# Kernel optimization log

Hardware: AMD Instinct MI355X
Metric: run time of the kernel (lower is better)

## Reference

```python
import jax, jax.numpy as jnp
import numpy as np

PATCH = 3
ALPHA = 0.5
EPS = 1e-12  # F.normalize default eps


def _unfold(x, p):
    # nn.Unfold(kernel_size=p, padding=p//2) then reshape(B, C, p*p, H*W)
    B, C, H, W = x.shape
    pad = p // 2
    xp = jnp.pad(x, ((0, 0), (0, 0), (pad, pad), (pad, pad)))
    # kernel positions row-major, matching torch unfold channel-major layout
    pats = jnp.stack([xp[:, :, i:i + H, j:j + W]
                      for i in range(p) for j in range(p)], axis=2)  # [B,C,K,H,W]
    return pats.reshape(B, C, p * p, H * W)


def setup_inputs() -> dict:
    key = jax.random.key(0)
    k1, k2 = jax.random.split(key)
    B, C, H, W = 4, 32, 256, 256
    fe_lv = jax.random.normal(k1, (B, C, H, W), dtype=jnp.float32)
    fused_features = jax.random.normal(k2, (B, C, H, W), dtype=jnp.float32)
    return {"fe_lv": fe_lv, "fused_features": fused_features}


def reference(fe_lv, fused_features):
    B, C, H, W = fe_lv.shape
    N = H * W
    patches = _unfold(fused_features, PATCH)          # [B,C,K,N]
    fe_flat = fe_lv.reshape(B, C, N)                  # [B,C,N]

    # cosine similarity over channel dim
    pn = patches / jnp.maximum(jnp.linalg.norm(patches, axis=1, keepdims=True), EPS)
    fn = fe_flat / jnp.maximum(jnp.linalg.norm(fe_flat, axis=1, keepdims=True), EPS)
    cosine_sim = jnp.einsum('bckn,bcn->bnk', pn, fn)  # [B,N,K]
    cosine_weights = jax.nn.softmax(cosine_sim, axis=-1)

    # euclidean distance over channel dim
    dist = jnp.sqrt(jnp.sum((patches - fe_flat[:, :, None, :]) ** 2, axis=1))  # [B,K,N]
    euclidean_weights = jax.nn.softmax(-dist.transpose(0, 2, 1), axis=-1)      # [B,N,K]

    weights = ALPHA * cosine_weights + (1.0 - ALPHA) * euclidean_weights
    refined = jnp.einsum('bnk,bckn->bcn', weights, patches)  # [B,C,N]
    return refined.reshape(B, C, H, W) + fe_lv
```

## Files before the change

kernel.cpp:

```cpp
#include <hip/hip_runtime.h>
#include <math.h>

#define B_ 4
#define C_ 32
#define H_ 256
#define W_ 256
#define HW_ (H_ * W_)
#define K_ 9
#define TX 32
#define TY 4
#define HX 34
#define HY 6
#define HCH (HX * HY)
#define NOCT 4
#define EPS_ 1e-12f

typedef _Float16 h2v __attribute__((ext_vector_type(2)));
typedef _Float16 h8v __attribute__((ext_vector_type(8)));

#if defined(__has_builtin)
#if __has_builtin(__builtin_amdgcn_fdot2)
#define HAVE_FDOT2 1
#endif
#if __has_builtin(__builtin_amdgcn_cvt_pkrtz)
#define HAVE_PKRTZ 1
#endif
#endif

static __device__ __forceinline__ h2v pk2(float a, float b) {
#if defined(HAVE_PKRTZ)
    return __builtin_bit_cast(h2v, __builtin_amdgcn_cvt_pkrtz(a, b));
#else
    h2v r = {(_Float16)a, (_Float16)b};
    return r;
#endif
}

static __device__ __forceinline__ float dot2(h2v a, h2v b, float c) {
#if defined(HAVE_FDOT2)
    return __builtin_amdgcn_fdot2(a, b, c, false);
#else
    return c + (float)a[0] * (float)b[0] + (float)a[1] * (float)b[1];
#endif
}

__global__ __launch_bounds__(256, 6) void asfr_kernel(const float* __restrict__ fe,
                                                      const float* __restrict__ fu,
                                                      float* __restrict__ out) {
    __shared__ h8v lds8[NOCT * 256];
    const int t = threadIdx.x;
    const int bx = blockIdx.x & 7;
    const int by = (blockIdx.x >> 3) & 63;
    const int b  = blockIdx.x >> 9;
    const int w0 = bx * TX, h0 = by * TY;

    const int x = t & 31;
    const int half = (t >> 5) & 1;
    const int y = t >> 6;
    const int c0 = half << 4;
    const int pxoff = b * (C_ * HW_) + (h0 + y) * W_ + (w0 + x);

    int goff[4];
    float msk[4];
#pragma unroll
    for (int j = 0; j < 4; ++j) {
        int u = t + j * 256;
        int oct = u >> 8;
        int pos = u & 255;
        int pp = pos < HCH ? pos : HCH - 1;
        int r = pp / HX;
        int col = pp - r * HX;
        int hh = h0 - 1 + r;
        int ww = w0 - 1 + col;
        bool ok = (pos < HCH) && ((unsigned)hh < (unsigned)H_) && ((unsigned)ww < (unsigned)W_);
        int hcl = hh < 0 ? 0 : (hh > H_ - 1 ? H_ - 1 : hh);
        int wcl = ww < 0 ? 0 : (ww > W_ - 1 ? W_ - 1 : ww);
        goff[j] = (oct * 8) * HW_ + hcl * W_ + wcl;
        msk[j] = ok ? 1.f : 0.f;
    }

    float fv[16];
#pragma unroll
    for (int cc = 0; cc < 16; ++cc) fv[cc] = fe[pxoff + (c0 + cc) * HW_];
    h8v fe8[2];
#pragma unroll
    for (int j = 0; j < 2; ++j)
#pragma unroll
        for (int c = 0; c < 4; ++c) {
            h2v p = pk2(fv[8 * j + 2 * c], fv[8 * j + 2 * c + 1]);
            fe8[j][2 * c] = p[0];
            fe8[j][2 * c + 1] = p[1];
        }

    const float* fub = fu + b * (C_ * HW_);
    float s[32];
#pragma unroll
    for (int j = 0; j < 4; ++j)
#pragma unroll
        for (int c = 0; c < 8; ++c) s[8 * j + c] = fub[goff[j] + c * HW_];
#pragma unroll
    for (int j = 0; j < 4; ++j) {
        h8v hv;
#pragma unroll
        for (int c = 0; c < 4; ++c) {
            h2v p = pk2(s[8 * j + 2 * c] * msk[j], s[8 * j + 2 * c + 1] * msk[j]);
            hv[2 * c] = p[0];
            hv[2 * c + 1] = p[1];
        }
        lds8[t + j * 256] = hv;
    }
    __syncthreads();

    const int hc = (y + 1) * HX + (x + 1);
    const int koff[K_] = {-HX - 1, -HX, -HX + 1, -1, 0, 1, HX - 1, HX, HX + 1};

    float dot[K_], psq[K_];
#pragma unroll
    for (int k = 0; k < K_; ++k) { dot[k] = 0.f; psq[k] = 0.f; }
    float fsq = 0.f;

#pragma unroll
    for (int j = 0; j < 2; ++j) {
        const int oct = 2 * half + j;
        h8v fq = fe8[j];
        h2v fA0 = __builtin_shufflevector(fq, fq, 0, 1);
        h2v fA1 = __builtin_shufflevector(fq, fq, 2, 3);
        h2v fA2 = __builtin_shufflevector(fq, fq, 4, 5);
        h2v fA3 = __builtin_shufflevector(fq, fq, 6, 7);
        fsq = dot2(fA0, fA0, fsq);
        fsq = dot2(fA1, fA1, fsq);
        fsq = dot2(fA2, fA2, fsq);
        fsq = dot2(fA3, fA3, fsq);
        const h8v* fubase = &lds8[(oct << 8) + hc];
#pragma unroll
        for (int k = 0; k < K_; ++k) {
            h8v p8 = fubase[koff[k]];
            h2v p0 = __builtin_shufflevector(p8, p8, 0, 1);
            h2v p1 = __builtin_shufflevector(p8, p8, 2, 3);
            h2v p2 = __builtin_shufflevector(p8, p8, 4, 5);
            h2v p3 = __builtin_shufflevector(p8, p8, 6, 7);
            dot[k] = dot2(p0, fA0, dot[k]);
            dot[k] = dot2(p1, fA1, dot[k]);
            dot[k] = dot2(p2, fA2, dot[k]);
            dot[k] = dot2(p3, fA3, dot[k]);
            psq[k] = dot2(p0, p0, psq[k]);
            psq[k] = dot2(p1, p1, psq[k]);
            psq[k] = dot2(p2, p2, psq[k]);
            psq[k] = dot2(p3, p3, psq[k]);
        }
    }

#pragma unroll
    for (int k = 0; k < K_; ++k) {
        dot[k] += __shfl_xor(dot[k], 32);
        psq[k] += __shfl_xor(psq[k], 32);
    }
    fsq += __shfl_xor(fsq, 32);

    float nf = fmaxf(sqrtf(fsq), EPS_);
    float cosv[K_], negd[K_];
#pragma unroll
    for (int k = 0; k < K_; ++k) {
        float np = fmaxf(sqrtf(psq[k]), EPS_);
        cosv[k] = __fdividef(dot[k], np * nf);
        float dsq = fmaxf(psq[k] - 2.f * dot[k] + fsq, 0.f);
        negd[k] = -sqrtf(dsq);
    }

    float m1 = cosv[0], m2 = negd[0];
#pragma unroll
    for (int k = 1; k < K_; ++k) { m1 = fmaxf(m1, cosv[k]); m2 = fmaxf(m2, negd[k]); }
    float s1 = 0.f, s2 = 0.f, e1[K_], e2[K_];
#pragma unroll
    for (int k = 0; k < K_; ++k) {
        e1[k] = __expf(cosv[k] - m1);
        e2[k] = __expf(negd[k] - m2);
        s1 += e1[k]; s2 += e2[k];
    }
    float r1 = __fdividef(0.5f, s1), r2 = __fdividef(0.5f, s2);
    h2v w2[K_];
#pragma unroll
    for (int k = 0; k < K_; ++k) {
        float wk = fmaf(e1[k], r1, e2[k] * r2);
        _Float16 wh = (_Float16)wk;
        h2v tmp = {wh, wh};
        w2[k] = tmp;
    }

#pragma unroll
    for (int j = 0; j < 2; ++j) {
        const int oct = 2 * half + j;
        const h8v* fubase = &lds8[(oct << 8) + hc];
        h2v a0 = {(_Float16)0, (_Float16)0};
        h2v a1 = a0, a2 = a0, a3 = a0;
#pragma unroll
        for (int k = 0; k < K_; ++k) {
            h8v p8 = fubase[koff[k]];
            a0 += w2[k] * __builtin_shufflevector(p8, p8, 0, 1);
            a1 += w2[k] * __builtin_shufflevector(p8, p8, 2, 3);
            a2 += w2[k] * __builtin_shufflevector(p8, p8, 4, 5);
            a3 += w2[k] * __builtin_shufflevector(p8, p8, 6, 7);
        }
        h8v fq = fe8[j];
        const int cg = oct * 8;
        out[pxoff + (cg + 0) * HW_] = (float)(fq[0] + a0[0]);
        out[pxoff + (cg + 1) * HW_] = (float)(fq[1] + a0[1]);
        out[pxoff + (cg + 2) * HW_] = (float)(fq[2] + a1[0]);
        out[pxoff + (cg + 3) * HW_] = (float)(fq[3] + a1[1]);
        out[pxoff + (cg + 4) * HW_] = (float)(fq[4] + a2[0]);
        out[pxoff + (cg + 5) * HW_] = (float)(fq[5] + a2[1]);
        out[pxoff + (cg + 6) * HW_] = (float)(fq[6] + a3[0]);
        out[pxoff + (cg + 7) * HW_] = (float)(fq[7] + a3[1]);
    }
}

extern "C" void kernel_launch(void* const* d_in, const int* in_sizes, int n_in,
                              void* d_out, int out_size, void* d_ws, size_t ws_size,
                              hipStream_t stream) {
    const float* fe = (const float*)d_in[0];
    const float* fu = (const float*)d_in[1];
    float* out = (float*)d_out;
    dim3 grid((W_ / TX) * (H_ / TY) * B_), block(256);
    hipLaunchKernelGGL(asfr_kernel, grid, block, 0, stream, fe, fu, out);
}
```

Before: 32.07 us.

## Precompute per-pixel patch squared norms in LDS and use rsqrt for cosine

Each halo pixel's squared norm over all 32 channels is computed once in fp32 while staging, stored in a shared buffer, and read back for the 9 neighbours. This removes the per-neighbour psq dot2 accumulation and its cross-half shuffle. The halo load is reorganized so each thread fetches all 32 channels of one spatial position, and the fe norm is computed in fp32. Cosine normalization now uses a single rsqrt of the product of squared norms instead of two sqrts and a divide. The cost is slightly different epsilon clamping and extra LDS space.

```diff
diff --git a/kernel.cpp b/kernel.cpp
--- a/kernel.cpp
+++ b/kernel.cpp
@@ -25,6 +25,13 @@
 #if __has_builtin(__builtin_amdgcn_cvt_pkrtz)
 #define HAVE_PKRTZ 1
 #endif
+#if __has_builtin(__builtin_amdgcn_rsqf)
+#define RSQ(xx) __builtin_amdgcn_rsqf(xx)
+#else
+#define RSQ(xx) (1.0f / sqrtf(xx))
+#endif
+#else
+#define RSQ(xx) (1.0f / sqrtf(xx))
 #endif
 
 static __device__ __forceinline__ h2v pk2(float a, float b) {
@@ -48,6 +55,7 @@
                                                       const float* __restrict__ fu,
                                                       float* __restrict__ out) {
     __shared__ h8v lds8[NOCT * 256];
+    __shared__ float sqb[256];
     const int t = threadIdx.x;
     const int bx = blockIdx.x & 7;
     const int by = (blockIdx.x >> 3) & 63;
@@ -60,13 +68,10 @@
     const int c0 = half << 4;
     const int pxoff = b * (C_ * HW_) + (h0 + y) * W_ + (w0 + x);
 
-    int goff[4];
-    float msk[4];
-#pragma unroll
-    for (int j = 0; j < 4; ++j) {
-        int u = t + j * 256;
-        int oct = u >> 8;
-        int pos = u & 255;
+    int spat;
+    float msk;
+    {
+        int pos = t;
         int pp = pos < HCH ? pos : HCH - 1;
         int r = pp / HX;
         int col = pp - r * HX;
@@ -75,13 +80,38 @@
         bool ok = (pos < HCH) && ((unsigned)hh < (unsigned)H_) && ((unsigned)ww < (unsigned)W_);
         int hcl = hh < 0 ? 0 : (hh > H_ - 1 ? H_ - 1 : hh);
         int wcl = ww < 0 ? 0 : (ww > W_ - 1 ? W_ - 1 : ww);
-        goff[j] = (oct * 8) * HW_ + hcl * W_ + wcl;
-        msk[j] = ok ? 1.f : 0.f;
-    }
+        spat = hcl * W_ + wcl;
+        msk = ok ? 1.f : 0.f;
+    }
+
+    const float* fub = fu + b * (C_ * HW_);
+    float s[32];
+#pragma unroll
+    for (int c = 0; c < 32; ++c) s[c] = fub[c * HW_ + spat];
 
     float fv[16];
 #pragma unroll
     for (int cc = 0; cc < 16; ++cc) fv[cc] = fe[pxoff + (c0 + cc) * HW_];
+
+    float part = 0.f;
+#pragma unroll
+    for (int c = 0; c < 32; ++c) part = fmaf(s[c], s[c], part);
+    sqb[t] = msk * part;
+#pragma unroll
+    for (int j = 0; j < 4; ++j) {
+        h8v hv;
+#pragma unroll
+        for (int c = 0; c < 4; ++c) {
+            h2v p = pk2(s[8 * j + 2 * c] * msk, s[8 * j + 2 * c + 1] * msk);
+            hv[2 * c] = p[0];
+            hv[2 * c + 1] = p[1];
+        }
+        lds8[t + j * 256] = hv;
+    }
+
+    float fsq = 0.f;
+#pragma unroll
+    for (int cc = 0; cc < 16; ++cc) fsq = fmaf(fv[cc], fv[cc], fsq);
     h8v fe8[2];
 #pragma unroll
     for (int j = 0; j < 2; ++j)
@@ -91,33 +121,18 @@
             fe8[j][2 * c] = p[0];
             fe8[j][2 * c + 1] = p[1];
         }
-
-    const float* fub = fu + b * (C_ * HW_);
-    float s[32];
-#pragma unroll
-    for (int j = 0; j < 4; ++j)
-#pragma unroll
-        for (int c = 0; c < 8; ++c) s[8 * j + c] = fub[goff[j] + c * HW_];
-#pragma unroll
-    for (int j = 0; j < 4; ++j) {
-        h8v hv;
-#pragma unroll
-        for (int c = 0; c < 4; ++c) {
-            h2v p = pk2(s[8 * j + 2 * c] * msk[j], s[8 * j + 2 * c + 1] * msk[j]);
-            hv[2 * c] = p[0];
-            hv[2 * c + 1] = p[1];
-        }
-        lds8[t + j * 256] = hv;
-    }
     __syncthreads();
 
     const int hc = (y + 1) * HX + (x + 1);
     const int koff[K_] = {-HX - 1, -HX, -HX + 1, -1, 0, 1, HX - 1, HX, HX + 1};
 
-    float dot[K_], psq[K_];
-#pragma unroll
-    for (int k = 0; k < K_; ++k) { dot[k] = 0.f; psq[k] = 0.f; }
-    float fsq = 0.f;
+    float psq[K_];
+#pragma unroll
+    for (int k = 0; k < K_; ++k) psq[k] = sqb[hc + koff[k]];
+
+    float dot[K_];
+#pragma unroll
+    for (int k = 0; k < K_; ++k) dot[k] = 0.f;
 
 #pragma unroll
     for (int j = 0; j < 2; ++j) {
@@ -127,42 +142,26 @@
         h2v fA1 = __builtin_shufflevector(fq, fq, 2, 3);
         h2v fA2 = __builtin_shufflevector(fq, fq, 4, 5);
         h2v fA3 = __builtin_shufflevector(fq, fq, 6, 7);
-        fsq = dot2(fA0, fA0, fsq);
-        fsq = dot2(fA1, fA1, fsq);
-        fsq = dot2(fA2, fA2, fsq);
-        fsq = dot2(fA3, fA3, fsq);
         const h8v* fubase = &lds8[(oct << 8) + hc];
 #pragma unroll
         for (int k = 0; k < K_; ++k) {
             h8v p8 = fubase[koff[k]];
-            h2v p0 = __builtin_shufflevector(p8, p8, 0, 1);
-            h2v p1 = __builtin_shufflevector(p8, p8, 2, 3);
-            h2v p2 = __builtin_shufflevector(p8, p8, 4, 5);
-            h2v p3 = __builtin_shufflevector(p8, p8, 6, 7);
-            dot[k] = dot2(p0, fA0, dot[k]);
-            dot[k] = dot2(p1, fA1, dot[k]);
-            dot[k] = dot2(p2, fA2, dot[k]);
-            dot[k] = dot2(p3, fA3, dot[k]);
-            psq[k] = dot2(p0, p0, psq[k]);
-            psq[k] = dot2(p1, p1, psq[k]);
-            psq[k] = dot2(p2, p2, psq[k]);
-            psq[k] = dot2(p3, p3, psq[k]);
-        }
-    }
-
+            dot[k] = dot2(__builtin_shufflevector(p8, p8, 0, 1), fA0, dot[k]);
+            dot[k] = dot2(__builtin_shufflevector(p8, p8, 2, 3), fA1, dot[k]);
+            dot[k] = dot2(__builtin_shufflevector(p8, p8, 4, 5), fA2, dot[k]);
+            dot[k] = dot2(__builtin_shufflevector(p8, p8, 6, 7), fA3, dot[k]);
+        }
+    }
+
+#pragma unroll
+    for (int k = 0; k < K_; ++k) dot[k] += __shfl_xor(dot[k], 32);
+    fsq += __shfl_xor(fsq, 32);
+
+    float cosv[K_], negd[K_];
 #pragma unroll
     for (int k = 0; k < K_; ++k) {
-        dot[k] += __shfl_xor(dot[k], 32);
-        psq[k] += __shfl_xor(psq[k], 32);
-    }
-    fsq += __shfl_xor(fsq, 32);
-
-    float nf = fmaxf(sqrtf(fsq), EPS_);
-    float cosv[K_], negd[K_];
-#pragma unroll
-    for (int k = 0; k < K_; ++k) {
-        float np = fmaxf(sqrtf(psq[k]), EPS_);
-        cosv[k] = __fdividef(dot[k], np * nf);
+        float prod = fmaxf(psq[k] * fsq, 1e-24f);
+        cosv[k] = dot[k] * RSQ(prod);
         float dsq = fmaxf(psq[k] - 2.f * dot[k] + fsq, 0.f);
         negd[k] = -sqrtf(dsq);
     }
```

New measurement: 34.69 us. 8.2% more time.
